# Kernel tuning notes

Measured on AMD Instinct MI355X. Metric: run time of the kernel, lower is better.

## Reference

```python
import jax, jax.numpy as jnp
import numpy as np

NUM_HEADS = 16
ROPE_THETA = 10000.0


def setup_inputs() -> dict:
    key = jax.random.key(0)
    k1, k2, k3 = jax.random.split(key, 3)
    B, T, C = 2, 2048, 1024
    x = jax.random.normal(k1, (B, T, C), dtype=jnp.float32)
    w_qkv = jax.random.normal(k2, (3 * C, C), dtype=jnp.float32) * 0.02
    w_out = jax.random.normal(k3, (C, C), dtype=jnp.float32) * 0.02
    return {"x": x, "w_qkv": w_qkv, "w_out": w_out}


def _apply_rope(x, cos, sin):
    # x: (B, H, T, D); interleaved complex pairs: (x[...,2i], x[...,2i+1])
    B, H, T, D = x.shape
    xp = x.reshape(B, H, T, D // 2, 2)
    xr, xi = xp[..., 0], xp[..., 1]
    # cos/sin: (T, D//2) broadcast over (B, H)
    out_r = xr * cos - xi * sin
    out_i = xr * sin + xi * cos
    return jnp.stack([out_r, out_i], axis=-1).reshape(B, H, T, D)


def reference(x, w_qkv, w_out):
    B, T, C = x.shape
    H = NUM_HEADS
    D = C // H
    scale = 1.0 / np.sqrt(D).astype(np.float32)

    qkv = x @ w_qkv.T                      # (B, T, 3C)
    q, k, v = jnp.split(qkv, 3, axis=-1)

    def to_heads(t):
        return t.reshape(B, T, H, D).transpose(0, 2, 1, 3)  # (B, H, T, D)

    q, k, v = to_heads(q), to_heads(k), to_heads(v)

    # RoPE frequencies: freqs[t, j] = t / theta^(2j/D)
    inv_freq = 1.0 / (ROPE_THETA ** (jnp.arange(0, D, 2, dtype=jnp.float32) / D))
    freqs = jnp.arange(T, dtype=jnp.float32)[:, None] * inv_freq[None, :]  # (T, D//2)
    cos, sin = jnp.cos(freqs), jnp.sin(freqs)

    q = _apply_rope(q, cos, sin)
    k = _apply_rope(k, cos, sin)

    att = jnp.einsum('bhqd,bhkd->bhqk', q, k) * scale   # (B, H, T, T)
    causal = jnp.tril(jnp.ones((T, T), dtype=bool))
    att = jnp.where(causal[None, None], att, -jnp.inf)
    att = jax.nn.softmax(att, axis=-1)
    # dropout p=0.0 (eval) -> identity

    out = jnp.einsum('bhqk,bhkd->bhqd', att, v)          # (B, H, T, D)
    out = out.transpose(0, 2, 1, 3).reshape(B, T, C)
    return out @ w_out.T
```

## Files before the change

### kernel.cpp

```cpp
#include <hip/hip_runtime.h>
#include <hip/hip_bf16.h>
#include <math.h>

#define DEV __device__ __forceinline__

typedef float  floatx4 __attribute__((ext_vector_type(4)));
typedef short  bf16x8  __attribute__((ext_vector_type(8)));
typedef short  bf16x4  __attribute__((ext_vector_type(4)));

typedef __attribute__((address_space(1))) void gvoid;
typedef __attribute__((address_space(3))) void lvoid;

static constexpr int Bc = 2, Tc = 2048, Cc = 1024, Hc = 16, Dc = 64;

DEV void gload16(const void* g, void* l) {
    __builtin_amdgcn_global_load_lds((gvoid*)g, (lvoid*)l, 16, 0, 0);
}

__global__ void prep_kernel(const float* __restrict__ xf,
                            const float* __restrict__ wqkvf,
                            const float* __restrict__ woutf,
                            __hip_bfloat16* __restrict__ xb,
                            __hip_bfloat16* __restrict__ wqkvb,
                            __hip_bfloat16* __restrict__ woutb,
                            float* __restrict__ cosT, float* __restrict__ sinT) {
    int gb = blockIdx.x;
    if (gb < 8192) {
        const float* src; __hip_bfloat16* dst; int i;
        if (gb < 4096)      { src = xf;    dst = xb;    i = gb * 256 + threadIdx.x; }
        else if (gb < 7168) { src = wqkvf; dst = wqkvb; i = (gb - 4096) * 256 + threadIdx.x; }
        else                { src = woutf; dst = woutb; i = (gb - 7168) * 256 + threadIdx.x; }
        float4 f = ((const float4*)src)[i];
        union { ushort4 u; __hip_bfloat16 h[4]; } pk;
        pk.h[0] = __float2bfloat16(f.x);
        pk.h[1] = __float2bfloat16(f.y);
        pk.h[2] = __float2bfloat16(f.z);
        pk.h[3] = __float2bfloat16(f.w);
        ((ushort4*)dst)[i] = pk.u;
    } else {
        int i = (gb - 8192) * 256 + threadIdx.x;
        int j = i >> 11, t = i & 2047;
        float invf = powf(10000.0f, -(float)j / 32.0f);
        float f = (float)t * invf;
        cosT[i] = cosf(f);
        sinT[i] = sinf(f);
    }
}

__global__ __launch_bounds__(256, 2) void gemm_qkv(
    const __hip_bfloat16* __restrict__ A,
    const __hip_bfloat16* __restrict__ Bm,
    __hip_bfloat16* __restrict__ qb,
    __hip_bfloat16* __restrict__ kb,
    __hip_bfloat16* __restrict__ vb,
    const float* __restrict__ cosT,
    const float* __restrict__ sinT,
    int K)
{
    __shared__ __align__(16) __hip_bfloat16 SM[2 * 128 * 64];
    __hip_bfloat16* const As = SM;
    __hip_bfloat16* const Bs = SM + 128 * 64;

    const int tid  = threadIdx.x;
    const int lane = tid & 63, wave = tid >> 6;
    const int quad = lane >> 4, cidx = lane & 15;
    const int wm = wave & 1, wn = wave >> 1;
    const int bm = blockIdx.x * 128, bn = blockIdx.y * 128;

    floatx4 acc[4][4] = {};

    for (int k0 = 0; k0 < K; k0 += 64) {
#pragma unroll
        for (int it = 0; it < 4; ++it) {
            int idx = tid + it * 256;
            int r = idx >> 3, cs = idx & 7;
            int cg = cs ^ (r & 7);
            gload16(A  + (size_t)(bm + r) * K + k0 + cg * 8, As + idx * 8);
            gload16(Bm + (size_t)(bn + r) * K + k0 + cg * 8, Bs + idx * 8);
        }
        __syncthreads();
#pragma unroll
        for (int ks = 0; ks < 2; ++ks) {
            bf16x8 af[4], bf[4];
#pragma unroll
            for (int mt = 0; mt < 4; ++mt) {
                int r = wm * 64 + mt * 16 + cidx;
                af[mt] = *(const bf16x8*)(As + (r * 8 + ((ks * 4 + quad) ^ (r & 7))) * 8);
            }
#pragma unroll
            for (int nt = 0; nt < 4; ++nt) {
                int r = wn * 64 + nt * 16 + cidx;
                bf[nt] = *(const bf16x8*)(Bs + (r * 8 + ((ks * 4 + quad) ^ (r & 7))) * 8);
            }
#pragma unroll
            for (int mt = 0; mt < 4; ++mt)
#pragma unroll
                for (int nt = 0; nt < 4; ++nt)
                    acc[mt][nt] = __builtin_amdgcn_mfma_f32_16x16x32_bf16(
                        af[mt], bf[nt], acc[mt][nt], 0, 0, 0);
        }
        __syncthreads();
    }

    if (bn >= 2048) {
#pragma unroll
        for (int nt = 0; nt < 4; ++nt) {
            int n_l = wn * 64 + nt * 16 + cidx;
#pragma unroll
            for (int mt = 0; mt < 4; ++mt)
#pragma unroll
                for (int reg = 0; reg < 4; ++reg) {
                    int m_l = wm * 64 + mt * 16 + quad * 4 + reg;
                    SM[n_l * 128 + (((m_l >> 3) ^ (n_l & 15)) * 8) + (m_l & 7)] =
                        __float2bfloat16(acc[mt][nt][reg]);
                }
        }
        __syncthreads();
        {
            int b = bm >> 11, t0 = bm & 2047;
            int c = tid & 15;
#pragma unroll
            for (int it = 0; it < 8; ++it) {
                int row = it * 16 + (tid >> 4);
                int cc = (bn - 2048) + row;
                int h = cc >> 6, d = cc & 63;
                *(uint4*)(vb + ((size_t)(b * Hc + h) * Dc + d) * Tc + t0 + c * 8) =
                    *(const uint4*)(SM + row * 128 + ((c ^ (row & 15)) * 8));
            }
        }
    } else {
        const float SL2E = 0.125f * 1.44269504088896f;
        const bool isq = (bn < 1024);
#pragma unroll
        for (int nt = 0; nt < 4; ++nt) {
            int n_l = wn * 64 + nt * 16 + cidx;
            int d = n_l & 63, j = d >> 1;
            const float* cp = cosT + j * 2048;
            const float* sp = sinT + j * 2048;
#pragma unroll
            for (int mt = 0; mt < 4; ++mt) {
                int m0 = wm * 64 + mt * 16 + quad * 4;
                int t0 = (bm + m0) & 2047;
                float4 c4 = *(const float4*)(cp + t0);
                float4 s4 = *(const float4*)(sp + t0);
#pragma unroll
                for (int reg = 0; reg < 4; ++reg) {
                    float v = acc[mt][nt][reg];
                    float p = __shfl_xor(v, 1);
                    float cz = ((const float*)&c4)[reg];
                    float sz = ((const float*)&s4)[reg];
                    float o = (d & 1) ? (p * sz + v * cz) : (v * cz - p * sz);
                    if (isq) o *= SL2E;
                    int m_l = m0 + reg;
                    SM[m_l * 128 + (((n_l >> 3) ^ (m_l & 15)) * 8) + (n_l & 7)] =
                        __float2bfloat16(o);
                }
            }
        }
        __syncthreads();
        {
            __hip_bfloat16* dst = isq ? qb : kb;
            const int bnl = bn & 1023;
#pragma unroll
            for (int it = 0; it < 8; ++it) {
                int c = it * 256 + tid;
                int row = c >> 4, s = c & 15;
                int m = bm + row;
                int b = m >> 11, t = m & 2047;
                int h = (bnl >> 6) + (s >> 3);
                int d0 = (s & 7) * 8;
                *(uint4*)(dst + ((size_t)(b * Hc + h) * Tc + t) * Dc + d0) =
                    *(const uint4*)(SM + row * 128 + ((s ^ (row & 15)) * 8));
            }
        }
    }
}

__global__ __launch_bounds__(256, 2) void gemm_out(
    const __hip_bfloat16* __restrict__ A,
    const __hip_bfloat16* __restrict__ Bm,
    float* __restrict__ Cout)
{
    __shared__ __align__(16) __hip_bfloat16 As[64 * 64];
    __shared__ __align__(16) __hip_bfloat16 Bs[128 * 64];

    const int tid  = threadIdx.x;
    const int lane = tid & 63, wave = tid >> 6;
    const int quad = lane >> 4, cidx = lane & 15;
    const int bm = blockIdx.x * 64, bn = blockIdx.y * 128;
    const int K = 1024;

    floatx4 acc[4][2] = {};

    for (int k0 = 0; k0 < K; k0 += 64) {
        int h = k0 >> 6;
#pragma unroll
        for (int it = 0; it < 2; ++it) {
            int idx = tid + it * 256;
            int r = idx >> 3, cs = idx & 7;
            int cg = cs ^ (r & 7);
            int m = bm + r;
            const __hip_bfloat16* src =
                A + ((size_t)((m >> 11) * 16 + h) * 2048 + (m & 2047)) * 64 + cg * 8;
            gload16(src, As + idx * 8);
        }
#pragma unroll
        for (int it = 0; it < 4; ++it) {
            int idx = tid + it * 256;
            int r = idx >> 3, cs = idx & 7;
            int cg = cs ^ (r & 7);
            gload16(Bm + (size_t)(bn + r) * K + k0 + cg * 8, Bs + idx * 8);
        }
        __syncthreads();
#pragma unroll
        for (int ks = 0; ks < 2; ++ks) {
            bf16x8 af[4], bf[2];
#pragma unroll
            for (int mt = 0; mt < 4; ++mt) {
                int r = mt * 16 + cidx;
                af[mt] = *(const bf16x8*)(As + (r * 8 + ((ks * 4 + quad) ^ (r & 7))) * 8);
            }
#pragma unroll
            for (int nt = 0; nt < 2; ++nt) {
                int r = wave * 32 + nt * 16 + cidx;
                bf[nt] = *(const bf16x8*)(Bs + (r * 8 + ((ks * 4 + quad) ^ (r & 7))) * 8);
            }
#pragma unroll
            for (int mt = 0; mt < 4; ++mt)
#pragma unroll
                for (int nt = 0; nt < 2; ++nt)
                    acc[mt][nt] = __builtin_amdgcn_mfma_f32_16x16x32_bf16(
                        af[mt], bf[nt], acc[mt][nt], 0, 0, 0);
        }
        __syncthreads();
    }

#pragma unroll
    for (int mt = 0; mt < 4; ++mt)
#pragma unroll
        for (int nt = 0; nt < 2; ++nt) {
            int n = bn + wave * 32 + nt * 16 + cidx;
#pragma unroll
            for (int reg = 0; reg < 4; ++reg) {
                int m = bm + mt * 16 + quad * 4 + reg;
                Cout[(size_t)m * 1024 + n] = acc[mt][nt][reg];
            }
        }
}

__global__ __launch_bounds__(256, 2) void attn_kernel(
    const __hip_bfloat16* __restrict__ qb,
    const __hip_bfloat16* __restrict__ kb,
    const __hip_bfloat16* __restrict__ vb,
    __hip_bfloat16* __restrict__ ob)
{
    __shared__ __align__(16) __hip_bfloat16 Ks[128 * 64];
    __shared__ __align__(16) __hip_bfloat16 Vt[64 * 128];
    __shared__ __align__(16) __hip_bfloat16 Ps[128 * 64];
    __shared__ float Ls[4][64];

    const int tid  = threadIdx.x;
    const int lane = tid & 63, wave = tid >> 6;
    const int quad = lane >> 4, cidx = lane & 15;
    const int id = blockIdx.x;
    const int xcd = id & 7, s = id >> 3;
    const int bh = xcd * 4 + (s >> 4);
    const int bx = s & 15;
    const size_t plane = (size_t)bh * Tc * Dc;
    const __hip_bfloat16* Vp = vb + plane;
    const __hip_bfloat16* Kp = kb + plane;

    for (int half = 0; half < 2; ++half) {
        const int qt = half ? bx : 31 - bx;
        const int qbase = qt * 64;
        const int ktmax = (qbase + 63) >> 7;

#pragma unroll
        for (int it = 0; it < 2; ++it) {
            int idx = tid + it * 256;
            int r = idx >> 3, cs = idx & 7;
            int cg = cs ^ (r & 7);
            gload16(qb + plane + (size_t)(qbase + r) * 64 + cg * 8, Ks + idx * 8);
        }
        __syncthreads();
        bf16x8 qf[4][2];
#pragma unroll
        for (int mt = 0; mt < 4; ++mt)
#pragma unroll
            for (int ks = 0; ks < 2; ++ks) {
                int r = mt * 16 + cidx;
                qf[mt][ks] = *(const bf16x8*)(Ks + (r * 8 + ((ks * 4 + quad) ^ (r & 7))) * 8);
            }
        __syncthreads();

        floatx4 oaccT[4][4] = {};
        float lsum[4] = {0.f, 0.f, 0.f, 0.f};

        for (int kt = 0; kt <= ktmax; ++kt) {
            bf16x8 kcur[2][2];
#pragma unroll
            for (int nt2 = 0; nt2 < 2; ++nt2)
#pragma unroll
                for (int ks = 0; ks < 2; ++ks)
                    kcur[nt2][ks] = *(const bf16x8*)(
                        Kp + (size_t)(kt * 128 + wave * 32 + nt2 * 16 + cidx) * 64
                           + (ks * 4 + quad) * 8);

#pragma unroll
            for (int it = 0; it < 4; ++it) {
                int idx = tid + it * 256;
                int r = idx >> 4, cs = idx & 15;
                int c = cs ^ (r & 15);
                gload16(Vp + (size_t)r * Tc + kt * 128 + c * 8, Vt + idx * 8);
            }

            floatx4 sacc[4][2] = {};
#pragma unroll
            for (int ks = 0; ks < 2; ++ks)
#pragma unroll
                for (int mt = 0; mt < 4; ++mt)
#pragma unroll
                    for (int nt2 = 0; nt2 < 2; ++nt2)
                        sacc[mt][nt2] = __builtin_amdgcn_mfma_f32_16x16x32_bf16(
                            kcur[nt2][ks], qf[mt][ks], sacc[mt][nt2], 0, 0, 0);

            const bool domask = (kt == ktmax);
            bf16x4 pf[4][2];
#pragma unroll
            for (int mt = 0; mt < 4; ++mt) {
                int q = qbase + mt * 16 + cidx;
#pragma unroll
                for (int nt2 = 0; nt2 < 2; ++nt2) {
#pragma unroll
                    for (int reg = 0; reg < 4; ++reg) {
                        int key = kt * 128 + wave * 32 + nt2 * 16 + quad * 4 + reg;
                        float p = __builtin_amdgcn_exp2f(sacc[mt][nt2][reg]);
                        if (domask && key > q) p = 0.0f;
                        lsum[mt] += p;
                        __hip_bfloat16 hb = __float2bfloat16(p);
                        pf[mt][nt2][reg] = *(const short*)&hb;
                    }
                }
            }

            __syncthreads();

#pragma unroll
            for (int dt = 0; dt < 4; ++dt) {
                int d = dt * 16 + cidx;
#pragma unroll
                for (int ks2 = 0; ks2 < 2; ++ks2) {
                    int chunk = wave * 4 + ks2 * 2 + (quad >> 1);
                    bf16x4 vtf = *(const bf16x4*)(
                        Vt + (d * 16 + (chunk ^ (d & 15))) * 8 + (quad & 1) * 4);
#pragma unroll
                    for (int mt = 0; mt < 4; ++mt)
                        oaccT[mt][dt] = __builtin_amdgcn_mfma_f32_16x16x16bf16_1k(
                            vtf, pf[mt][ks2], oaccT[mt][dt], 0, 0, 0);
                }
            }
            __syncthreads();
        }

#pragma unroll
        for (int off = 16; off < 64; off <<= 1)
#pragma unroll
            for (int mt = 0; mt < 4; ++mt)
                lsum[mt] += __shfl_xor(lsum[mt], off);
        if (quad == 0)
#pragma unroll
            for (int mt = 0; mt < 4; ++mt)
                Ls[wave][mt * 16 + cidx] = lsum[mt];

        if (wave != 0) {
            float* dstw = (wave == 1) ? (float*)Ks : (wave == 2) ? (float*)Vt : (float*)Ps;
#pragma unroll
            for (int mt = 0; mt < 4; ++mt)
#pragma unroll
                for (int dt = 0; dt < 4; ++dt)
                    ((floatx4*)dstw)[(mt * 4 + dt) * 64 + lane] = oaccT[mt][dt];
        }
        __syncthreads();
        if (wave == 0) {
#pragma unroll
            for (int mt = 0; mt < 4; ++mt)
#pragma unroll
                for (int dt = 0; dt < 4; ++dt) {
                    int i = (mt * 4 + dt) * 64 + lane;
                    oaccT[mt][dt] += ((const floatx4*)Ks)[i];
                    oaccT[mt][dt] += ((const floatx4*)Vt)[i];
                    oaccT[mt][dt] += ((const floatx4*)Ps)[i];
                }
#pragma unroll
            for (int mt = 0; mt < 4; ++mt) {
                int q = mt * 16 + cidx;
                float lt = Ls[0][q] + Ls[1][q] + Ls[2][q] + Ls[3][q];
                float inv = 1.0f / lt;
#pragma unroll
                for (int dt = 0; dt < 4; ++dt) {
                    bf16x4 o4;
#pragma unroll
                    for (int reg = 0; reg < 4; ++reg) {
                        __hip_bfloat16 hb = __float2bfloat16(oaccT[mt][dt][reg] * inv);
                        o4[reg] = *(const short*)&hb;
                    }
                    int g = dt * 4 + quad;
                    *(bf16x4*)(Ps + q * 64 + (g ^ (q & 12)) * 4) = o4;
                }
            }
        }
        __syncthreads();
#pragma unroll
        for (int i = 0; i < 2; ++i) {
            int c = tid * 2 + i;
            int row = c >> 3, cp = c & 7;
            *(uint4*)(ob + plane + (size_t)(qbase + row) * 64 + cp * 8) =
                *(const uint4*)(Ps + row * 64 + ((cp * 2) ^ (row & 12)) * 4);
        }
        __syncthreads();
    }
}

extern "C" void kernel_launch(void* const* d_in, const int* in_sizes, int n_in,
                              void* d_out, int out_size, void* d_ws, size_t ws_size,
                              hipStream_t stream) {
    const float* xf = nullptr; const float* wqkvf = nullptr; const float* woutf = nullptr;
    for (int i = 0; i < n_in; ++i) {
        if      (in_sizes[i] == 2 * 2048 * 1024) xf    = (const float*)d_in[i];
        else if (in_sizes[i] == 3 * 1024 * 1024) wqkvf = (const float*)d_in[i];
        else if (in_sizes[i] == 1024 * 1024)     woutf = (const float*)d_in[i];
    }
    float* out = (float*)d_out;

    char* ws = (char*)d_ws;
    const size_t MB = 1024 * 1024;
    __hip_bfloat16* qb    = (__hip_bfloat16*)(ws);
    __hip_bfloat16* kb    = (__hip_bfloat16*)(ws + 8  * MB);
    __hip_bfloat16* vb    = (__hip_bfloat16*)(ws + 16 * MB);
    __hip_bfloat16* ab    = (__hip_bfloat16*)(ws + 24 * MB);
    float* cosT           = (float*)(ws + 32 * MB);
    float* sinT           = (float*)(ws + 32 * MB + 256 * 1024);
    __hip_bfloat16* xb    = (__hip_bfloat16*)(ws + 33 * MB);
    __hip_bfloat16* wqkvb = (__hip_bfloat16*)(ws + 41 * MB);
    __hip_bfloat16* woutb = (__hip_bfloat16*)(ws + 47 * MB);

    prep_kernel<<<dim3(8448), dim3(256), 0, stream>>>(
        xf, wqkvf, woutf, xb, wqkvb, woutb, cosT, sinT);

    gemm_qkv<<<dim3(32, 24), dim3(256), 0, stream>>>(
        xb, wqkvb, qb, kb, vb, cosT, sinT, 1024);
    attn_kernel<<<dim3(512), dim3(256), 0, stream>>>(qb, kb, vb, ab);
    gemm_out<<<dim3(64, 8), dim3(256), 0, stream>>>(ab, woutb, out);
}
```

Measured before the change: 161.6 us.

## Double-buffer V tiles and prefetch next K fragments in attention loop

```diff
diff --git a/kernel.cpp b/kernel.cpp
--- a/kernel.cpp
+++ b/kernel.cpp
@@ -282,6 +282,21 @@
             int cg = cs ^ (r & 7);
             gload16(qb + plane + (size_t)(qbase + r) * 64 + cg * 8, Ks + idx * 8);
         }
+#pragma unroll
+        for (int it = 0; it < 4; ++it) {
+            int idx = tid + it * 256;
+            int r = idx >> 4, cs = idx & 15;
+            int c = cs ^ (r & 15);
+            gload16(Vp + (size_t)r * Tc + 0 * 128 + c * 8, Vt + idx * 8);
+        }
+        bf16x8 kcur[2][2];
+#pragma unroll
+        for (int nt2 = 0; nt2 < 2; ++nt2)
+#pragma unroll
+            for (int ks = 0; ks < 2; ++ks)
+                kcur[nt2][ks] = *(const bf16x8*)(
+                    Kp + (size_t)(wave * 32 + nt2 * 16 + cidx) * 64
+                       + (ks * 4 + quad) * 8);
         __syncthreads();
         bf16x8 qf[4][2];
 #pragma unroll
@@ -297,21 +312,24 @@
         float lsum[4] = {0.f, 0.f, 0.f, 0.f};
 
         for (int kt = 0; kt <= ktmax; ++kt) {
-            bf16x8 kcur[2][2];
-#pragma unroll
-            for (int nt2 = 0; nt2 < 2; ++nt2)
-#pragma unroll
-                for (int ks = 0; ks < 2; ++ks)
-                    kcur[nt2][ks] = *(const bf16x8*)(
-                        Kp + (size_t)(kt * 128 + wave * 32 + nt2 * 16 + cidx) * 64
-                           + (ks * 4 + quad) * 8);
-
-#pragma unroll
-            for (int it = 0; it < 4; ++it) {
-                int idx = tid + it * 256;
-                int r = idx >> 4, cs = idx & 15;
-                int c = cs ^ (r & 15);
-                gload16(Vp + (size_t)r * Tc + kt * 128 + c * 8, Vt + idx * 8);
+            const bool more = (kt < ktmax);
+            bf16x8 knxt[2][2];
+            if (more) {
+#pragma unroll
+                for (int nt2 = 0; nt2 < 2; ++nt2)
+#pragma unroll
+                    for (int ks = 0; ks < 2; ++ks)
+                        knxt[nt2][ks] = *(const bf16x8*)(
+                            Kp + (size_t)((kt + 1) * 128 + wave * 32 + nt2 * 16 + cidx) * 64
+                               + (ks * 4 + quad) * 8);
+                __hip_bfloat16* vdst = ((kt + 1) & 1) ? Ps : Vt;
+#pragma unroll
+                for (int it = 0; it < 4; ++it) {
+                    int idx = tid + it * 256;
+                    int r = idx >> 4, cs = idx & 15;
+                    int c = cs ^ (r & 15);
+                    gload16(Vp + (size_t)r * Tc + (kt + 1) * 128 + c * 8, vdst + idx * 8);
+                }
             }
 
             floatx4 sacc[4][2] = {};
@@ -343,8 +361,13 @@
                 }
             }
 
-            __syncthreads();
-
+            __builtin_amdgcn_sched_barrier(0);
+            if (more) { asm volatile("s_waitcnt vmcnt(8)" ::: "memory"); }
+            else      { asm volatile("s_waitcnt vmcnt(0)" ::: "memory"); }
+            __builtin_amdgcn_s_barrier();
+            __builtin_amdgcn_sched_barrier(0);
+
+            const __hip_bfloat16* vcur = (kt & 1) ? Ps : Vt;
 #pragma unroll
             for (int dt = 0; dt < 4; ++dt) {
                 int d = dt * 16 + cidx;
@@ -352,14 +375,25 @@
                 for (int ks2 = 0; ks2 < 2; ++ks2) {
                     int chunk = wave * 4 + ks2 * 2 + (quad >> 1);
                     bf16x4 vtf = *(const bf16x4*)(
-                        Vt + (d * 16 + (chunk ^ (d & 15))) * 8 + (quad & 1) * 4);
+                        vcur + (d * 16 + (chunk ^ (d & 15))) * 8 + (quad & 1) * 4);
 #pragma unroll
                     for (int mt = 0; mt < 4; ++mt)
                         oaccT[mt][dt] = __builtin_amdgcn_mfma_f32_16x16x16bf16_1k(
                             vtf, pf[mt][ks2], oaccT[mt][dt], 0, 0, 0);
                 }
             }
-            __syncthreads();
+
+            __builtin_amdgcn_sched_barrier(0);
+            __builtin_amdgcn_s_barrier();
+            __builtin_amdgcn_sched_barrier(0);
+
+            if (more) {
+#pragma unroll
+                for (int nt2 = 0; nt2 < 2; ++nt2)
+#pragma unroll
+                    for (int ks = 0; ks < 2; ++ks)
+                        kcur[nt2][ks] = knxt[nt2][ks];
+            }
         }
 
 #pragma unroll
```

Result: slower. 170.1 us (+5.3%).

## Split attention work by query rows per wave and double-buffer K/V tiles

Applied to the files above, without the earlier changes.

```diff
diff --git a/kernel.cpp b/kernel.cpp
--- a/kernel.cpp
+++ b/kernel.cpp
@@ -254,10 +254,9 @@
     const __hip_bfloat16* __restrict__ vb,
     __hip_bfloat16* __restrict__ ob)
 {
-    __shared__ __align__(16) __hip_bfloat16 Ks[128 * 64];
-    __shared__ __align__(16) __hip_bfloat16 Vt[64 * 128];
-    __shared__ __align__(16) __hip_bfloat16 Ps[128 * 64];
-    __shared__ float Ls[4][64];
+    __shared__ __align__(16) __hip_bfloat16 Kb[2 * 128 * 64];
+    __shared__ __align__(16) __hip_bfloat16 Vb[2 * 64 * 128];
+    __shared__ __align__(16) __hip_bfloat16 Os[64 * 64];
 
     const int tid  = threadIdx.x;
     const int lane = tid & 63, wave = tid >> 6;
@@ -278,135 +277,114 @@
 #pragma unroll
         for (int it = 0; it < 2; ++it) {
             int idx = tid + it * 256;
-            int r = idx >> 3, cs = idx & 7;
-            int cg = cs ^ (r & 7);
-            gload16(qb + plane + (size_t)(qbase + r) * 64 + cg * 8, Ks + idx * 8);
-        }
-        __syncthreads();
-        bf16x8 qf[4][2];
-#pragma unroll
-        for (int mt = 0; mt < 4; ++mt)
-#pragma unroll
-            for (int ks = 0; ks < 2; ++ks) {
-                int r = mt * 16 + cidx;
-                qf[mt][ks] = *(const bf16x8*)(Ks + (r * 8 + ((ks * 4 + quad) ^ (r & 7))) * 8);
-            }
-        __syncthreads();
-
-        floatx4 oaccT[4][4] = {};
-        float lsum[4] = {0.f, 0.f, 0.f, 0.f};
+            int r = idx >> 3, cg = (idx & 7) ^ (r & 7);
+            gload16(qb + plane + (size_t)(qbase + r) * 64 + cg * 8, Os + idx * 8);
+        }
+#pragma unroll
+        for (int it = 0; it < 4; ++it) {
+            int idx = tid + it * 256;
+            int r = idx >> 3, cg = (idx & 7) ^ (r & 7);
+            gload16(Kp + (size_t)r * 64 + cg * 8, Kb + idx * 8);
+        }
+#pragma unroll
+        for (int it = 0; it < 4; ++it) {
+            int idx = tid + it * 256;
+            int r = idx >> 4, c = (idx & 15) ^ (r & 15);
+            gload16(Vp + (size_t)r * Tc + c * 8, Vb + idx * 8);
+        }
+        __syncthreads();
+
+        bf16x8 qf[2];
+#pragma unroll
+        for (int ks = 0; ks < 2; ++ks) {
+            int r = wave * 16 + cidx;
+            qf[ks] = *(const bf16x8*)(Os + (r * 8 + ((ks * 4 + quad) ^ (r & 7))) * 8);
+        }
+
+        floatx4 oaccT[4] = {};
+        float lsum = 0.0f;
+        const int q = qbase + wave * 16 + cidx;
 
         for (int kt = 0; kt <= ktmax; ++kt) {
-            bf16x8 kcur[2][2];
-#pragma unroll
-            for (int nt2 = 0; nt2 < 2; ++nt2)
-#pragma unroll
-                for (int ks = 0; ks < 2; ++ks)
-                    kcur[nt2][ks] = *(const bf16x8*)(
-                        Kp + (size_t)(kt * 128 + wave * 32 + nt2 * 16 + cidx) * 64
-                           + (ks * 4 + quad) * 8);
-
-#pragma unroll
-            for (int it = 0; it < 4; ++it) {
-                int idx = tid + it * 256;
-                int r = idx >> 4, cs = idx & 15;
-                int c = cs ^ (r & 15);
-                gload16(Vp + (size_t)r * Tc + kt * 128 + c * 8, Vt + idx * 8);
-            }
-
-            floatx4 sacc[4][2] = {};
+            const __hip_bfloat16* Kc = Kb + (kt & 1) * (128 * 64);
+            const __hip_bfloat16* Vc = Vb + (kt & 1) * (64 * 128);
+
+            if (kt < ktmax) {
+                __hip_bfloat16* Kn = Kb + ((kt + 1) & 1) * (128 * 64);
+                __hip_bfloat16* Vn = Vb + ((kt + 1) & 1) * (64 * 128);
+#pragma unroll
+                for (int it = 0; it < 4; ++it) {
+                    int idx = tid + it * 256;
+                    int r = idx >> 3, cg = (idx & 7) ^ (r & 7);
+                    gload16(Kp + (size_t)((kt + 1) * 128 + r) * 64 + cg * 8, Kn + idx * 8);
+                }
+#pragma unroll
+                for (int it = 0; it < 4; ++it) {
+                    int idx = tid + it * 256;
+                    int r = idx >> 4, c = (idx & 15) ^ (r & 15);
+                    gload16(Vp + (size_t)r * Tc + (kt + 1) * 128 + c * 8, Vn + idx * 8);
+                }
+            }
+
+            floatx4 sacc[8] = {};
 #pragma unroll
             for (int ks = 0; ks < 2; ++ks)
 #pragma unroll
-                for (int mt = 0; mt < 4; ++mt)
-#pragma unroll
-                    for (int nt2 = 0; nt2 < 2; ++nt2)
-                        sacc[mt][nt2] = __builtin_amdgcn_mfma_f32_16x16x32_bf16(
-                            kcur[nt2][ks], qf[mt][ks], sacc[mt][nt2], 0, 0, 0);
+                for (int kb2 = 0; kb2 < 8; ++kb2) {
+                    int r = kb2 * 16 + cidx;
+                    bf16x8 af = *(const bf16x8*)(
+                        Kc + (r * 8 + ((ks * 4 + quad) ^ (r & 7))) * 8);
+                    sacc[kb2] = __builtin_amdgcn_mfma_f32_16x16x32_bf16(
+                        af, qf[ks], sacc[kb2], 0, 0, 0);
+                }
 
             const bool domask = (kt == ktmax);
-            bf16x4 pf[4][2];
-#pragma unroll
-            for (int mt = 0; mt < 4; ++mt) {
-                int q = qbase + mt * 16 + cidx;
-#pragma unroll
-                for (int nt2 = 0; nt2 < 2; ++nt2) {
-#pragma unroll
-                    for (int reg = 0; reg < 4; ++reg) {
-                        int key = kt * 128 + wave * 32 + nt2 * 16 + quad * 4 + reg;
-                        float p = __builtin_amdgcn_exp2f(sacc[mt][nt2][reg]);
-                        if (domask && key > q) p = 0.0f;
-                        lsum[mt] += p;
-                        __hip_bfloat16 hb = __float2bfloat16(p);
-                        pf[mt][nt2][reg] = *(const short*)&hb;
-                    }
-                }
-            }
-
-            __syncthreads();
+            bf16x4 pf[8];
+#pragma unroll
+            for (int kb2 = 0; kb2 < 8; ++kb2) {
+#pragma unroll
+                for (int reg = 0; reg < 4; ++reg) {
+                    int key = kt * 128 + kb2 * 16 + quad * 4 + reg;
+                    float p = __builtin_amdgcn_exp2f(sacc[kb2][reg]);
+                    if (domask && key > q) p = 0.0f;
+                    lsum += p;
+                    __hip_bfloat16 hb = __float2bfloat16(p);
+                    pf[kb2][reg] = *(const short*)&hb;
+                }
+            }
 
 #pragma unroll
             for (int dt = 0; dt < 4; ++dt) {
                 int d = dt * 16 + cidx;
 #pragma unroll
-                for (int ks2 = 0; ks2 < 2; ++ks2) {
-                    int chunk = wave * 4 + ks2 * 2 + (quad >> 1);
+                for (int c8 = 0; c8 < 8; ++c8) {
+                    int ch = c8 * 2 + (quad >> 1);
                     bf16x4 vtf = *(const bf16x4*)(
-                        Vt + (d * 16 + (chunk ^ (d & 15))) * 8 + (quad & 1) * 4);
-#pragma unroll
-                    for (int mt = 0; mt < 4; ++mt)
-                        oaccT[mt][dt] = __builtin_amdgcn_mfma_f32_16x16x16bf16_1k(
-                            vtf, pf[mt][ks2], oaccT[mt][dt], 0, 0, 0);
-                }
-            }
+                        Vc + (d * 16 + (ch ^ (d & 15))) * 8 + (quad & 1) * 4);
+                    oaccT[dt] = __builtin_amdgcn_mfma_f32_16x16x16bf16_1k(
+                        vtf, pf[c8], oaccT[dt], 0, 0, 0);
+                }
+            }
+
             __syncthreads();
         }
 
-#pragma unroll
-        for (int off = 16; off < 64; off <<= 1)
-#pragma unroll
-            for (int mt = 0; mt < 4; ++mt)
-                lsum[mt] += __shfl_xor(lsum[mt], off);
-        if (quad == 0)
-#pragma unroll
-            for (int mt = 0; mt < 4; ++mt)
-                Ls[wave][mt * 16 + cidx] = lsum[mt];
-
-        if (wave != 0) {
-            float* dstw = (wave == 1) ? (float*)Ks : (wave == 2) ? (float*)Vt : (float*)Ps;
-#pragma unroll
-            for (int mt = 0; mt < 4; ++mt)
-#pragma unroll
-                for (int dt = 0; dt < 4; ++dt)
-                    ((floatx4*)dstw)[(mt * 4 + dt) * 64 + lane] = oaccT[mt][dt];
-        }
-        __syncthreads();
-        if (wave == 0) {
-#pragma unroll
-            for (int mt = 0; mt < 4; ++mt)
-#pragma unroll
-                for (int dt = 0; dt < 4; ++dt) {
-                    int i = (mt * 4 + dt) * 64 + lane;
-                    oaccT[mt][dt] += ((const floatx4*)Ks)[i];
-                    oaccT[mt][dt] += ((const floatx4*)Vt)[i];
-                    oaccT[mt][dt] += ((const floatx4*)Ps)[i];
-                }
-#pragma unroll
-            for (int mt = 0; mt < 4; ++mt) {
-                int q = mt * 16 + cidx;
-                float lt = Ls[0][q] + Ls[1][q] + Ls[2][q] + Ls[3][q];
-                float inv = 1.0f / lt;
-#pragma unroll
-                for (int dt = 0; dt < 4; ++dt) {
-                    bf16x4 o4;
-#pragma unroll
-                    for (int reg = 0; reg < 4; ++reg) {
-                        __hip_bfloat16 hb = __float2bfloat16(oaccT[mt][dt][reg] * inv);
-                        o4[reg] = *(const short*)&hb;
-                    }
-                    int g = dt * 4 + quad;
-                    *(bf16x4*)(Ps + q * 64 + (g ^ (q & 12)) * 4) = o4;
-                }
+        float l = lsum;
+        l += __shfl_xor(l, 16);
+        l += __shfl_xor(l, 32);
+        float inv = 1.0f / l;
+        {
+            int qq = wave * 16 + cidx;
+#pragma unroll
+            for (int dt = 0; dt < 4; ++dt) {
+                bf16x4 o4;
+#pragma unroll
+                for (int reg = 0; reg < 4; ++reg) {
+                    __hip_bfloat16 hb = __float2bfloat16(oaccT[dt][reg] * inv);
+                    o4[reg] = *(const short*)&hb;
+                }
+                int g = dt * 4 + quad;
+                *(bf16x4*)(Os + qq * 64 + ((g ^ (qq & 12)) * 4)) = o4;
             }
         }
         __syncthreads();
@@ -415,7 +393,7 @@
             int c = tid * 2 + i;
             int row = c >> 3, cp = c & 7;
             *(uint4*)(ob + plane + (size_t)(qbase + row) * 64 + cp * 8) =
-                *(const uint4*)(Ps + row * 64 + ((cp * 2) ^ (row & 12)) * 4);
+                *(const uint4*)(Os + row * 64 + ((cp * 2) ^ (row & 12)) * 4);
         }
         __syncthreads();
     }
```

After: 166.7 us. +3.2%, slower.
